# Kernel tuning notes

Hardware: AMD Instinct MI355X
Metric: run time of the kernel (lower is better)

The kernel has to match this reference:

```python
import jax, jax.numpy as jnp
import numpy as np

# model constants (par dict in original repo)
U = 0.45
U_STD = -0.55
ALPHA_STD = 0.006667   # dt / tau_std
ALPHA_STF = 0.05       # dt / tau_stf
DT = 10.0              # ms
TAU_MEM = 100.0        # ms

N_INPUT, N_HIDDEN, N_OUTPUT = 64, 256, 16
BATCH, T = 16, 64


def setup_inputs() -> dict:
    key = jax.random.key(0)
    ks = jax.random.split(key, 4)
    x = jax.random.normal(ks[0], (T, BATCH, N_INPUT), dtype=jnp.float32)
    # orthogonal-ish init is irrelevant for correctness; scaled gaussians suffice
    W_in = jax.random.normal(ks[1], (N_INPUT, N_HIDDEN), dtype=jnp.float32) / np.sqrt(N_INPUT)
    W_rec = jax.random.normal(ks[2], (N_HIDDEN, N_HIDDEN), dtype=jnp.float32) / np.sqrt(N_HIDDEN)
    W_bias = jnp.zeros((N_HIDDEN,), dtype=jnp.float32)
    W_out = jax.random.normal(ks[3], (N_HIDDEN, N_OUTPUT), dtype=jnp.float32) / np.sqrt(N_HIDDEN)
    W_out_b = jnp.zeros((N_OUTPUT,), dtype=jnp.float32)
    return {"x": x, "W_in": W_in, "W_rec": W_rec, "W_bias": W_bias,
            "W_out": W_out, "W_out_b": W_out_b}


def reference(x, W_in, W_rec, W_bias, W_out, W_out_b):
    B = x.shape[1]
    H = W_rec.shape[0]
    dt_s = DT / 1000.0
    dtm = DT / TAU_MEM

    h0 = jnp.zeros((B, H), x.dtype)
    sx0 = jnp.ones((B, H, H), x.dtype)                 # syn_x init
    su0 = jnp.full((B, H, H), U_STD + 1.0, x.dtype)    # syn_u init = U_std + 1

    def step(carry, inp):
        h, sx, su = carry
        # syn_x update: uses OLD syn_u, syn_x, h; h broadcast over last axis (presyn index i)
        sx_new = sx + ALPHA_STD * (1.0 - sx) - dt_s * (su * sx) * h[:, :, None]
        # syn_u update: batched matmul (U*(1-su)) @ Hmat where Hmat[b,i,j] = h[b,i]
        # -> result[b,i,j] = sum_k (U*(1-su))[b,i,k] * h[b,k], constant over j
        v = jnp.einsum('bik,bk->bi', U * (1.0 - su), h)
        su_new = su + ALPHA_STF * (U - su) + dt_s * v[:, :, None]
        sx_new = jnp.clip(sx_new, 0.0, 1.0)
        su_new = jnp.clip(su_new, 0.0, 1.0)
        # hidden update: h @ (syn_x*syn_u*W_rec) as (B,1,H)x(B,H,H)
        rec = jnp.einsum('bi,bij->bj', h, (sx_new * su_new) * W_rec)
        h_new = jax.nn.relu((1.0 - dtm) * h + dtm * (rec + W_bias) + inp @ W_in)
        y = jax.nn.sigmoid(h_new @ W_out + W_out_b)
        return (h_new, sx_new, su_new), (h_new, y, sx_new, su_new)

    _, (h_seq, y_seq, sx_seq, su_seq) = jax.lax.scan(step, (h0, sx0, su0), x)
    # prepend initial states to mirror the original lists (T+1 states, T outputs)
    h_all = jnp.concatenate([h0[None], h_seq], axis=0)
    sx_all = jnp.concatenate([sx0[None], sx_seq], axis=0)
    su_all = jnp.concatenate([su0[None], su_seq], axis=0)
    return h_all, y_seq, sx_all, su_all
```

## Files before the change

kernel.cpp:

```cpp
#include <hip/hip_runtime.h>

typedef _Float16 half2_t __attribute__((ext_vector_type(2)));
typedef float float4_t __attribute__((ext_vector_type(4)));
typedef unsigned long long u64;

#define U_PAR 0.45f
#define A_STD 0.006667f
#define A_STF 0.05f
#define DT_S  0.01f

#define T_STEPS 64
#define BATCH   16
#define NIN     64
#define NH      256
#define NOUT    16

#define H_OFF  0
#define H_SZ   ((T_STEPS + 1) * BATCH * NH)
#define Y_OFF  H_SZ
#define Y_SZ   (T_STEPS * BATCH * NOUT)
#define SX_OFF (Y_OFF + Y_SZ)
#define PLANE  ((T_STEPS + 1) * BATCH * NH)
#define SX_SZ  ((size_t)PLANE * NH)
#define SU_OFF ((size_t)SX_OFF + SX_SZ)

#define GROUP    32
#define N_ROWS   (2 * PLANE)
#define N_GROUPS (N_ROWS / GROUP)
#define TAG_BASE 0x5EED0000u

static __device__ __forceinline__ float fdot2f(half2_t a, half2_t b, float c) {
#if __has_builtin(__builtin_amdgcn_fdot2)
  return __builtin_amdgcn_fdot2(a, b, c, false);
#else
  return c + (float)a.x * (float)b.x + (float)a.y * (float)b.y;
#endif
}

static __device__ __forceinline__ void bar_lds() {
  asm volatile("s_waitcnt lgkmcnt(0)" ::: "memory");
  __builtin_amdgcn_s_barrier();
  asm volatile("" ::: "memory");
}

__global__ __launch_bounds__(512, 4) void rnn_fused(
    const float* __restrict__ x, const float* __restrict__ Win,
    const float* __restrict__ Wrec, const float* __restrict__ Wbias,
    const float* __restrict__ Wout, const float* __restrict__ Woutb,
    float* __restrict__ out, u64* __restrict__ wsx64, u64* __restrict__ wsu64)
{
  __shared__ __align__(16) _Float16 g_h[NH];
  __shared__ __align__(16) _Float16 x16[T_STEPS][NIN];
  __shared__ __align__(16) _Float16 xw16[T_STEPS][NH];
  __shared__ float p_s[NH];
  __shared__ float red_s[4];
  __shared__ float sval[2][GROUP];

  if (blockIdx.x < BATCH) {
    __builtin_amdgcn_s_setprio(1);
    const int b    = blockIdx.x;
    const int tid  = threadIdx.x;
    const int j    = tid & 255;
    const int q    = tid >> 8;
    const int wv   = tid >> 6;
    const int lane = tid & 63;

#pragma unroll
    for (int e = 0; e < 8; ++e) {
      int idx = e * 512 + tid;
      int t = idx >> 6, i = idx & 63;
      x16[t][i] = (_Float16)x[(size_t)(t * BATCH + b) * NIN + i];
    }
    bar_lds();

    {
      half2_t win2[32];
#pragma unroll
      for (int k = 0; k < 32; ++k) {
        float a0 = Win[(2 * k) * NH + j];
        float a1 = Win[(2 * k + 1) * NH + j];
        half2_t v; v.x = (_Float16)a0; v.y = (_Float16)a1;
        win2[k] = v;
      }
      for (int tt = 0; tt < 32; ++tt) {
        int t = q * 32 + tt;
        const half2_t* x2 = (const half2_t*)x16[t];
        float xa0 = 0.f, xa1 = 0.f;
#pragma unroll
        for (int k = 0; k < 32; k += 2) {
          xa0 = fdot2f(win2[k], x2[k], xa0);
          xa1 = fdot2f(win2[k + 1], x2[k + 1], xa1);
        }
        xw16[t][j] = (_Float16)(xa0 + xa1);
      }
    }

    half2_t w2[64];
#pragma unroll
    for (int k = 0; k < 64; ++k) {
      float a0 = Wrec[(q * 128 + 2 * k) * NH + j];
      float a1 = Wrec[(q * 128 + 2 * k + 1) * NH + j];
      half2_t v; v.x = (_Float16)a0; v.y = (_Float16)a1;
      w2[k] = v;
    }
    const float bias = (q == 0) ? Wbias[j] : 0.f;

    float h = 0.f, sx = 1.f, su = U_PAR;
    if (q == 0) out[H_OFF + b * NH + j] = 0.f;
    bar_lds();

    for (int t = 0; t < T_STEPS; ++t) {
      if (q == 0) {
        float s = h;
#pragma unroll
        for (int m = 1; m < 64; m <<= 1) s += __shfl_xor(s, m, 64);
        if (lane == 0) red_s[wv] = s;
      }
      bar_lds();

      float xwv = 0.f;
      if (q == 0) {
        float S = red_s[0] + red_s[1] + red_s[2] + red_s[3];
        float sxn = sx + A_STD * (1.f - sx) - DT_S * su * sx * h;
        float sun = su + A_STF * (U_PAR - su) + DT_S * (U_PAR * (1.f - su) * S);
        sxn = fminf(fmaxf(sxn, 0.f), 1.f);
        sun = fminf(fmaxf(sun, 0.f), 1.f);
        g_h[j] = (_Float16)(h * sxn * sun);
        const int row = (t + 1) * BATCH + b;
        u64 tg = (u64)(TAG_BASE | (unsigned)row) << 32;
        __hip_atomic_store(&wsx64[(size_t)row * NH + j],
                           tg | (u64)__float_as_uint(sxn),
                           __ATOMIC_RELAXED, __HIP_MEMORY_SCOPE_AGENT);
        __hip_atomic_store(&wsu64[(size_t)row * NH + j],
                           tg | (u64)__float_as_uint(sun),
                           __ATOMIC_RELAXED, __HIP_MEMORY_SCOPE_AGENT);
        sx = sxn; su = sun;
        xwv = (float)xw16[t][j];
      }
      bar_lds();

      float a0 = 0.f, a1 = 0.f;
      {
        const half2_t* g2 = (const half2_t*)g_h + q * 64;
#pragma unroll
        for (int k = 0; k < 64; k += 2) {
          a0 = fdot2f(w2[k],     g2[k],     a0);
          a1 = fdot2f(w2[k + 1], g2[k + 1], a1);
        }
      }
      float partial = a0 + a1;
      if (q == 1) p_s[j] = partial;
      bar_lds();

      if (q == 0) {
        float rec = partial + p_s[j];
        float hn = fmaxf(0.9f * h + 0.1f * (rec + bias) + xwv, 0.f);
        out[H_OFF + (size_t)((t + 1) * BATCH + b) * NH + j] = hn;
        xw16[t][j] = (_Float16)hn;
        h = hn;
      }
    }

    bar_lds();
    {
      const int part = lane >> 4;
      const int o    = lane & 15;
      for (int tt = 0; tt < 8; ++tt) {
        int t = wv * 8 + tt;
        float acc = 0.f;
#pragma unroll 8
        for (int j2 = 0; j2 < 64; ++j2) {
          int jj = part * 64 + j2;
          acc = fmaf((float)xw16[t][jj], Wout[jj * NOUT + o], acc);
        }
        acc += __shfl_xor(acc, 16, 64);
        acc += __shfl_xor(acc, 32, 64);
        if (lane < NOUT) {
          out[Y_OFF + (size_t)(t * BATCH + b) * NOUT + lane] =
              1.f / (1.f + expf(-(acc + Woutb[lane])));
        }
      }
    }
    __builtin_amdgcn_s_setprio(0);
  } else {
    const int nCons = (int)gridDim.x - BATCH;
    const int cb    = (int)blockIdx.x - BATCH;
    const int tid   = threadIdx.x;

    auto stageFn = [&](int g, int buf) {
      int r0    = g * GROUP;
      int t     = r0 >> 13;
      int rem   = r0 & 8191;
      int which = rem >> 12;
      int b     = (rem >> 8) & 15;
      int i0    = rem & 255;
      if (t == 0) {
        sval[buf][tid] = which ? U_PAR : 1.0f;
        return;
      }
      int row = (t << 4) | b;
      unsigned exp = TAG_BASE | (unsigned)row;
      const u64* src = (which ? wsu64 : wsx64) + (size_t)row * NH + i0 + tid;
      u64 v = __hip_atomic_load(src, __ATOMIC_RELAXED, __HIP_MEMORY_SCOPE_AGENT);
      while ((unsigned)(v >> 32) != exp) {
        __builtin_amdgcn_s_sleep(32);
        v = __hip_atomic_load(src, __ATOMIC_RELAXED, __HIP_MEMORY_SCOPE_AGENT);
      }
      sval[buf][tid] = __uint_as_float((unsigned)(v & 0xFFFFFFFFu));
    };

    if (cb < N_GROUPS && tid < GROUP) stageFn(cb, 0);
    int k = 0;
    for (int g = cb; g < N_GROUPS; g += nCons, ++k) {
      int buf = k & 1;
      bar_lds();
      int gn = g + nCons;
      if (gn < N_GROUPS && tid < GROUP) stageFn(gn, buf ^ 1);

      int r0    = g * GROUP;
      int t     = r0 >> 13;
      int rem   = r0 & 8191;
      int which = rem >> 12;
      int b     = (rem >> 8) & 15;
      int i0    = rem & 255;
      size_t rowbase = (size_t)(((t << 4) | b) * NH + i0);
      float* dstBase = out + (which ? SU_OFF : (size_t)SX_OFF) + rowbase * NH;
#pragma unroll
      for (int p = 0; p < 4; ++p) {
        int id = p * 512 + tid;
        int rr = id >> 6, c = id & 63;
        float v = sval[buf][rr];
        float4_t f4 = {v, v, v, v};
        __builtin_nontemporal_store(f4, (float4_t*)(dstBase + (size_t)rr * NH) + c);
      }
    }
  }
}

__global__ __launch_bounds__(512) void rnn_phase1(
    const float* __restrict__ x, const float* __restrict__ Win,
    const float* __restrict__ Wrec, const float* __restrict__ Wbias,
    float* __restrict__ out)
{
  const int b   = blockIdx.x;
  const int tid = threadIdx.x;
  const int j   = tid & 255;
  const int q   = tid >> 8;

  __shared__ __align__(16) _Float16 g_h[NH];
  __shared__ __align__(16) _Float16 x_h[NIN];
  __shared__ float p_s[NH];
  __shared__ float xw_s[NH];
  __shared__ float red_s[8];

  half2_t w2[64];
#pragma unroll
  for (int k = 0; k < 64; ++k) {
    float a0 = Wrec[(q * 128 + 2 * k) * NH + j];
    float a1 = Wrec[(q * 128 + 2 * k + 1) * NH + j];
    half2_t v; v.x = (_Float16)a0; v.y = (_Float16)a1;
    w2[k] = v;
  }
  half2_t win2[32];
  if (q == 1) {
#pragma unroll
    for (int k = 0; k < 32; ++k) {
      float a0 = Win[(2 * k) * NH + j];
      float a1 = Win[(2 * k + 1) * NH + j];
      half2_t v; v.x = (_Float16)a0; v.y = (_Float16)a1;
      win2[k] = v;
    }
  }

  float h = 0.f, sx = 1.f, su = U_PAR;
  float bias = 0.f;
  if (q == 0) bias = Wbias[j];

  if (q == 0) {
    out[H_OFF + b * NH + j] = 0.f;
    size_t row0 = (size_t)b * NH + j;
    out[SX_OFF + row0 * NH] = 1.f;
    out[SU_OFF + row0 * NH] = U_PAR;
  }

  for (int t = 0; t < T_STEPS; ++t) {
    if (q == 0) {
      float s = h;
#pragma unroll
      for (int m = 1; m < 64; m <<= 1) s += __shfl_xor(s, m, 64);
      if ((tid & 63) == 0) red_s[tid >> 6] = s;
    } else {
      if (j < NIN) x_h[j] = (_Float16)x[(size_t)(t * BATCH + b) * NIN + j];
    }
    __syncthreads();

    float partial = 0.f;
    if (q == 0) {
      float S   = red_s[0] + red_s[1] + red_s[2] + red_s[3];
      float sxn = sx + A_STD * (1.f - sx) - DT_S * su * sx * h;
      float v   = U_PAR * (1.f - su) * S;
      float sun = su + A_STF * (U_PAR - su) + DT_S * v;
      sxn = fminf(fmaxf(sxn, 0.f), 1.f);
      sun = fminf(fmaxf(sun, 0.f), 1.f);
      float g = h * sxn * sun;
      g_h[j] = (_Float16)g;
      sx = sxn; su = sun;
      size_t row = (size_t)((t + 1) * BATCH + b) * NH + j;
      out[SX_OFF + row * NH] = sxn;
      out[SU_OFF + row * NH] = sun;
    } else {
      float xw = 0.f;
      const half2_t* x2 = (const half2_t*)x_h;
#pragma unroll
      for (int k = 0; k < 32; ++k) xw = fdot2f(win2[k], x2[k], xw);
      xw_s[j] = xw;
    }
    __syncthreads();

    {
      const half2_t* g2 = (const half2_t*)g_h;
#pragma unroll
      for (int k = 0; k < 64; ++k) partial = fdot2f(w2[k], g2[q * 64 + k], partial);
    }
    if (q == 1) p_s[j] = partial;
    __syncthreads();

    if (q == 0) {
      float rec = partial + p_s[j];
      float hn  = 0.9f * h + 0.1f * (rec + bias) + xw_s[j];
      hn = fmaxf(hn, 0.f);
      out[H_OFF + ((size_t)(t + 1) * BATCH + b) * NH + j] = hn;
      h = hn;
    }
  }
}

__global__ __launch_bounds__(256) void rnn_yhead(
    const float* __restrict__ Wout, const float* __restrict__ Woutb,
    float* __restrict__ out)
{
  const int tb = blockIdx.x;
  const int t  = tb / BATCH, b = tb % BATCH;
  const int j  = threadIdx.x;
  __shared__ float red[NOUT][5];

  float h = out[H_OFF + ((size_t)(t + 1) * BATCH + b) * NH + j];
  const float* wrow = Wout + j * NOUT;
#pragma unroll
  for (int o = 0; o < NOUT; ++o) {
    float v = h * wrow[o];
#pragma unroll
    for (int m = 1; m < 64; m <<= 1) v += __shfl_xor(v, m, 64);
    if ((j & 63) == 0) red[o][j >> 6] = v;
  }
  __syncthreads();
  if (j < NOUT) {
    float v = red[j][0] + red[j][1] + red[j][2] + red[j][3] + Woutb[j];
    out[Y_OFF + (size_t)tb * NOUT + j] = 1.f / (1.f + expf(-v));
  }
}

__global__ __launch_bounds__(256) void rnn_bcast(float* __restrict__ out)
{
  const size_t base = SX_OFF;
  const int ROWS = 32;
  __shared__ float sv[ROWS];
  const int ngroups = (2 * PLANE) / ROWS;
  for (int grp = blockIdx.x; grp < ngroups; grp += gridDim.x) {
    size_t r0 = (size_t)grp * ROWS;
    if (threadIdx.x < ROWS) sv[threadIdx.x] = out[base + (r0 + threadIdx.x) * NH];
    __syncthreads();
#pragma unroll
    for (int p = 0; p < 8; ++p) {
      int id = p * 256 + threadIdx.x;
      int r = id >> 6, c = id & 63;
      float v = sv[r];
      float4_t f4 = {v, v, v, v};
      float4_t* dst = (float4_t*)(out + base + (r0 + r) * NH);
      __builtin_nontemporal_store(f4, dst + c);
    }
    __syncthreads();
  }
}

extern "C" void kernel_launch(void* const* d_in, const int* in_sizes, int n_in,
                              void* d_out, int out_size, void* d_ws, size_t ws_size,
                              hipStream_t stream) {
  (void)in_sizes; (void)n_in; (void)out_size;
  const float* x     = (const float*)d_in[0];
  const float* Win   = (const float*)d_in[1];
  const float* Wrec  = (const float*)d_in[2];
  const float* Wbias = (const float*)d_in[3];
  const float* Wout  = (const float*)d_in[4];
  const float* Woutb = (const float*)d_in[5];
  float* out = (float*)d_out;

  const size_t WS_NEED = 2 * (size_t)PLANE * sizeof(u64);
  u64* wsx64 = (u64*)d_ws;
  u64* wsu64 = wsx64 + PLANE;

  bool coop_ok = (ws_size >= WS_NEED);
  int dev = 0, cus = 0, occ = 0;
  if (coop_ok && hipGetDevice(&dev) != hipSuccess) coop_ok = false;
  if (coop_ok && hipDeviceGetAttribute(&cus, hipDeviceAttributeMultiprocessorCount,
                                       dev) != hipSuccess) coop_ok = false;
  if (coop_ok && hipOccupancyMaxActiveBlocksPerMultiprocessor(
                     &occ, (const void*)rnn_fused, 512, 0) != hipSuccess) coop_ok = false;
  if (occ < 1) coop_ok = false;
  int grid = occ * cus;
  if (grid > BATCH + 2048) grid = BATCH + 2048;
  if (grid < 80) coop_ok = false;

  if (coop_ok) {
    void* args[] = {(void*)&x, (void*)&Win, (void*)&Wrec, (void*)&Wbias,
                    (void*)&Wout, (void*)&Woutb, (void*)&out,
                    (void*)&wsx64, (void*)&wsu64};
    hipError_t e = hipLaunchCooperativeKernel((const void*)rnn_fused, dim3(grid),
                                              dim3(512), args, 0, stream);
    if (e == hipSuccess) return;
  }

  hipLaunchKernelGGL(rnn_phase1, dim3(BATCH), dim3(512), 0, stream,
                     x, Win, Wrec, Wbias, out);
  hipLaunchKernelGGL(rnn_yhead, dim3(T_STEPS * BATCH), dim3(256), 0, stream,
                     Wout, Woutb, out);
  hipLaunchKernelGGL(rnn_bcast, dim3(2048), dim3(256), 0, stream, out);
}
```

Before: 123.4 us.

## Make consumer blocks work per-wavefront, dropping block barriers and LDS staging

The consumer path that broadcasts syn_x/syn_u rows into the large output planes now assigns each work group to a single wavefront instead of a whole block. Values travel through wave shuffles rather than LDS, which removes the per-group block barrier and the shared staging buffer. Each wave prefetches the next group's tagged value before it writes the current one. The spin sleep interval is also shortened, so waves poll faster. This lets independent waves proceed without waiting on the slowest wave in the block, at the cost of more polling traffic and a different store pattern per wave.

```diff
diff --git a/kernel.cpp b/kernel.cpp
--- a/kernel.cpp
+++ b/kernel.cpp
@@ -54,7 +54,6 @@
   __shared__ __align__(16) _Float16 xw16[T_STEPS][NH];
   __shared__ float p_s[NH];
   __shared__ float red_s[4];
-  __shared__ float sval[2][GROUP];
 
   if (blockIdx.x < BATCH) {
     __builtin_amdgcn_s_setprio(1);
@@ -184,55 +183,67 @@
     __builtin_amdgcn_s_setprio(0);
   } else {
     const int nCons = (int)gridDim.x - BATCH;
-    const int cb    = (int)blockIdx.x - BATCH;
     const int tid   = threadIdx.x;
-
-    auto stageFn = [&](int g, int buf) {
-      int r0    = g * GROUP;
-      int t     = r0 >> 13;
-      int rem   = r0 & 8191;
-      int which = rem >> 12;
-      int b     = (rem >> 8) & 15;
-      int i0    = rem & 255;
+    const int wv    = tid >> 6, lane = tid & 63;
+    const int nW    = nCons * 8;
+    const int g0    = ((int)blockIdx.x - BATCH) * 8 + wv;
+
+    auto params = [&](int g, int& t, int& which, int& row, int& i0) {
+      int r0 = g * GROUP;
+      t = r0 >> 13;
+      int rem = r0 & 8191;
+      which = rem >> 12;
+      int b2 = (rem >> 8) & 15;
+      i0 = rem & 255;
+      row = (t << 4) | b2;
+    };
+
+    u64 v = 0;
+    if (g0 < N_GROUPS) {
+      int t, which, row, i0;
+      params(g0, t, which, row, i0);
+      if (t != 0 && lane < GROUP)
+        v = __hip_atomic_load((which ? wsu64 : wsx64) + (size_t)row * NH + i0 + lane,
+                              __ATOMIC_RELAXED, __HIP_MEMORY_SCOPE_AGENT);
+    }
+
+    for (int g = g0; g < N_GROUPS; g += nW) {
+      int t, which, row, i0;
+      params(g, t, which, row, i0);
+      float val;
       if (t == 0) {
-        sval[buf][tid] = which ? U_PAR : 1.0f;
-        return;
-      }
-      int row = (t << 4) | b;
-      unsigned exp = TAG_BASE | (unsigned)row;
-      const u64* src = (which ? wsu64 : wsx64) + (size_t)row * NH + i0 + tid;
-      u64 v = __hip_atomic_load(src, __ATOMIC_RELAXED, __HIP_MEMORY_SCOPE_AGENT);
-      while ((unsigned)(v >> 32) != exp) {
-        __builtin_amdgcn_s_sleep(32);
-        v = __hip_atomic_load(src, __ATOMIC_RELAXED, __HIP_MEMORY_SCOPE_AGENT);
-      }
-      sval[buf][tid] = __uint_as_float((unsigned)(v & 0xFFFFFFFFu));
-    };
-
-    if (cb < N_GROUPS && tid < GROUP) stageFn(cb, 0);
-    int k = 0;
-    for (int g = cb; g < N_GROUPS; g += nCons, ++k) {
-      int buf = k & 1;
-      bar_lds();
-      int gn = g + nCons;
-      if (gn < N_GROUPS && tid < GROUP) stageFn(gn, buf ^ 1);
-
-      int r0    = g * GROUP;
-      int t     = r0 >> 13;
-      int rem   = r0 & 8191;
-      int which = rem >> 12;
-      int b     = (rem >> 8) & 15;
-      int i0    = rem & 255;
-      size_t rowbase = (size_t)(((t << 4) | b) * NH + i0);
-      float* dstBase = out + (which ? SU_OFF : (size_t)SX_OFF) + rowbase * NH;
-#pragma unroll
-      for (int p = 0; p < 4; ++p) {
-        int id = p * 512 + tid;
-        int rr = id >> 6, c = id & 63;
-        float v = sval[buf][rr];
-        float4_t f4 = {v, v, v, v};
-        __builtin_nontemporal_store(f4, (float4_t*)(dstBase + (size_t)rr * NH) + c);
-      }
+        val = which ? U_PAR : 1.0f;
+      } else {
+        unsigned exp = TAG_BASE | (unsigned)row;
+        const u64* src = (which ? wsu64 : wsx64) + (size_t)row * NH + i0 + lane;
+        if (lane < GROUP) {
+          while ((unsigned)(v >> 32) != exp) {
+            __builtin_amdgcn_s_sleep(8);
+            v = __hip_atomic_load(src, __ATOMIC_RELAXED, __HIP_MEMORY_SCOPE_AGENT);
+          }
+        }
+        val = __uint_as_float((unsigned)(v & 0xFFFFFFFFu));
+      }
+
+      int gn = g + nW;
+      u64 vn = 0;
+      if (gn < N_GROUPS) {
+        int tn, whichn, rown, i0n;
+        params(gn, tn, whichn, rown, i0n);
+        if (tn != 0 && lane < GROUP)
+          vn = __hip_atomic_load((whichn ? wsu64 : wsx64) + (size_t)rown * NH + i0n + lane,
+                                 __ATOMIC_RELAXED, __HIP_MEMORY_SCOPE_AGENT);
+      }
+
+      float* dstBase = out + (which ? SU_OFF : (size_t)SX_OFF)
+                       + ((size_t)row * NH + i0) * NH;
+#pragma unroll
+      for (int it = 0; it < GROUP; ++it) {
+        float vv = __shfl(val, it, 64);
+        float4_t f4 = {vv, vv, vv, vv};
+        __builtin_nontemporal_store(f4, (float4_t*)(dstBase + (size_t)it * NH) + lane);
+      }
+      v = vn;
     }
   }
 }
```

New measurement: 129.7 us. +5.1%, slower.
